# Optimization experiments

Measured on AMD Instinct MI355X. Metric: run time of the kernel, lower is better.

Reference implementation:

```python
import jax, jax.numpy as jnp
import numpy as np

WH, WW = 12, 12
NUM_HEADS = 8
NW = 4


def _relative_position_index():
    ch, cw = np.meshgrid(np.arange(WH), np.arange(WW), indexing='ij')
    coords = np.stack([ch, cw]).reshape(2, -1)            # [2, Wh*Ww]
    rel = coords[:, :, None] - coords[:, None, :]         # [2, M, M]
    rel = rel.transpose(1, 2, 0)                          # [M, M, 2]
    rel[:, :, 0] += WH - 1
    rel[:, :, 1] += WW - 1
    rel[:, :, 0] *= 2 * WW - 1
    return jnp.asarray(rel.sum(-1))                       # [M, M] int


def setup_inputs() -> dict:
    key = jax.random.key(0)
    ks = jax.random.split(key, 11)
    C = 512
    B_, N = 512, WH * WW + 1
    std = 0.02
    return {
        'x': jax.random.normal(ks[0], (B_, N, C), dtype=jnp.float32),
        'mask': jnp.zeros((NW, N, N), dtype=jnp.float32),
        'rpb_table': jax.random.normal(ks[1], ((2 * WH - 1) * (2 * WW - 1), NUM_HEADS), dtype=jnp.float32) * std,
        'Wq': jax.random.normal(ks[2], (C, C), dtype=jnp.float32) * (C ** -0.5),
        'bq': jax.random.normal(ks[3], (C,), dtype=jnp.float32) * std,
        'Wk': jax.random.normal(ks[4], (C, C), dtype=jnp.float32) * (C ** -0.5),
        'bk': jax.random.normal(ks[5], (C,), dtype=jnp.float32) * std,
        'Wv': jax.random.normal(ks[6], (C, C), dtype=jnp.float32) * (C ** -0.5),
        'bv': jax.random.normal(ks[7], (C,), dtype=jnp.float32) * std,
        'Wo': jax.random.normal(ks[8], (C, C), dtype=jnp.float32) * (C ** -0.5),
        'bo': jax.random.normal(ks[9], (C,), dtype=jnp.float32) * std,
    }


def reference(x, mask, rpb_table, Wq, bq, Wk, bk, Wv, bv, Wo, bo):
    B_, N, C = x.shape
    H = NUM_HEADS
    hd = C // H
    scale = hd ** -0.5
    B = B_ // NW
    M = WH * WW  # window tokens (N = M + 1 global token)

    def proj(W, b):
        return (x @ W.T + b).reshape(B_, N, H, hd).transpose(0, 2, 1, 3)  # [B_,H,N,hd]

    q = proj(Wq, bq)
    k = proj(Wk, bk)
    v = proj(Wv, bv)

    attn = jnp.einsum('bhnd,bhmd->bhnm', q, k) * scale  # [B_,H,N,N]

    rel_idx = _relative_position_index()                 # [M,M]
    bias = rpb_table[rel_idx].transpose(2, 0, 1)          # [H,M,M]
    attn = attn.at[:, :, :M, :M].add(bias[None])          # N != M: bias on window block only

    # shifted-window mask: (nW, N, N)
    attn = (attn.reshape(B, NW, H, N, N) + mask[None, :, None]).reshape(B_, H, N, N)

    # ---- global-token attention redistribution (gx) ----
    ga = attn[:, :, -1, :].reshape(B, NW, H, N).transpose(0, 2, 1, 3)   # [B,H,NW,N]
    g1 = ga[:, :, :, :M].reshape(B, H, NW * M)                           # window keys, all windows
    g2 = ga[:, :, :, M].mean(-1, keepdims=True)                          # mean global-global logit [B,H,1]
    g = jax.nn.softmax(jnp.concatenate([g1, g2], axis=-1), axis=-1)      # [B,H,NW*M+1]
    g1 = g[:, :, :-1].reshape(B, H, NW, M).transpose(0, 2, 1, 3).reshape(B_, H, M)
    g2 = jnp.broadcast_to(g[:, :, -1][:, None, :], (B, NW, H)).reshape(B_, H, 1)
    ga_full = jnp.concatenate([g1, g2], axis=-1)[:, :, None, :]          # [B_,H,1,N]
    gx = jnp.einsum('bhqn,bhnd->bhqd', ga_full, v).transpose(0, 2, 1, 3).reshape(B_, C)
    gx = gx.reshape(B, NW, C).sum(1)                                     # sum over windows [B,C]
    gx = jnp.broadcast_to(gx[:, None, :], (B, NW, C)).reshape(B_, C)

    # ---- standard window attention ----
    attn = jax.nn.softmax(attn, axis=-1)
    out = jnp.einsum('bhnm,bhmd->bhnd', attn, v).transpose(0, 2, 1, 3).reshape(B_, N, C)
    out = out.at[:, -1, :].set(gx)
    return out @ Wo.T + bo
```

## Files before the change

kernel.cpp:

```cpp
#include <hip/hip_runtime.h>
#include <hip/hip_bf16.h>
#include <stdint.h>

#define NTOK 145
#define MTOK 144
#define CDIM 512
#define NHEAD 8
#define HD 64
#define NWIN 4
#define BWIN 512
#define MROWS (BWIN*NTOK)

typedef short short8 __attribute__((ext_vector_type(8)));
typedef float f32x4 __attribute__((ext_vector_type(4)));

__device__ __forceinline__ uint16_t f2bf(float f) {
  union { float f; uint32_t u; } x; x.f = f;
  uint32_t r = x.u + 0x7FFFu + ((x.u >> 16) & 1u);
  return (uint16_t)(r >> 16);
}
__device__ __forceinline__ float bf2f(uint16_t u) {
  union { uint32_t u; float f; } x; x.u = ((uint32_t)u) << 16; return x.f;
}
__device__ __forceinline__ uint32_t pack2(float a, float b) {
  return (uint32_t)f2bf(a) | ((uint32_t)f2bf(b) << 16);
}

__global__ void prep_kernel(const float* __restrict__ rpb,
                            const float* __restrict__ Wq, const float* __restrict__ bq,
                            const float* __restrict__ Wk, const float* __restrict__ bk,
                            const float* __restrict__ Wv, const float* __restrict__ bv,
                            const float* __restrict__ Wo,
                            uint16_t* __restrict__ wqkv, uint16_t* __restrict__ wo,
                            float* __restrict__ bqkv, float* __restrict__ biastab) {
  int id = blockIdx.x * 256 + threadIdx.x;
  const int A = 1536*512, B = 512*512, C2 = 1536, D = 8*144*144;
  if (id < A) {
    int n = id >> 9, k = id & 511;
    const float* W = (n < 512) ? Wq : (n < 1024) ? Wk : Wv;
    wqkv[id] = f2bf(W[(size_t)(n & 511)*512 + k]);
  } else if ((id -= A) < B) {
    wo[id] = f2bf(Wo[id]);
  } else if ((id -= B) < C2) {
    bqkv[id] = (id < 512) ? bq[id] : (id < 1024) ? bk[id-512] : bv[id-1024];
  } else if ((id -= C2) < D) {
    int h = id / (144*144); int rr = id % (144*144);
    int i = rr / 144, j = rr % 144;
    int rel = (i/12 - j/12 + 11) * 23 + (i%12 - j%12 + 11);
    biastab[id] = rpb[rel*8 + h];
  }
}

__global__ __launch_bounds__(256) void gemm_qkv(
    const float* __restrict__ x, const uint16_t* __restrict__ wqkv,
    const float* __restrict__ bqkv,
    uint16_t* __restrict__ qb, uint16_t* __restrict__ kb, uint16_t* __restrict__ vb) {
  __shared__ __align__(16) uint16_t As[128*32];
  __shared__ __align__(16) uint16_t Bs[128*32];
  int bid = blockIdx.x;
  int mb = bid / 12, nb = bid % 12;
  int tid = threadIdx.x;
  int lane = tid & 63, w = tid >> 6;
  int wm = w >> 1, wn = w & 1;
  int lm = lane & 15, lq = lane >> 4;
  int sr = tid >> 1, sh = tid & 1;

  const float* agp = x + (size_t)(mb*128 + sr)*512 + sh*16;
  const uint16_t* bgp = wqkv + (size_t)(nb*128 + sr)*512 + sh*16;

  f32x4 acc[4][4];
#pragma unroll
  for (int a = 0; a < 4; a++)
#pragma unroll
    for (int b = 0; b < 4; b++) acc[a][b] = (f32x4){0.f,0.f,0.f,0.f};

  float4 af0 = *(const float4*)(agp+0), af1 = *(const float4*)(agp+4);
  float4 af2 = *(const float4*)(agp+8), af3 = *(const float4*)(agp+12);
  uint4 bu0 = *(const uint4*)(bgp), bu1 = *(const uint4*)(bgp+8);

  for (int kt = 0; kt < 16; kt++) {
    uint32_t p0 = pack2(af0.x, af0.y), p1 = pack2(af0.z, af0.w);
    uint32_t p2 = pack2(af1.x, af1.y), p3 = pack2(af1.z, af1.w);
    uint32_t p4 = pack2(af2.x, af2.y), p5 = pack2(af2.z, af2.w);
    uint32_t p6 = pack2(af3.x, af3.y), p7 = pack2(af3.z, af3.w);
    *(uint4*)&As[sr*32 + sh*16]     = make_uint4(p0,p1,p2,p3);
    *(uint4*)&As[sr*32 + sh*16 + 8] = make_uint4(p4,p5,p6,p7);
    *(uint4*)&Bs[sr*32 + sh*16]     = bu0;
    *(uint4*)&Bs[sr*32 + sh*16 + 8] = bu1;
    __syncthreads();
    if (kt < 15) {
      const float* ag = agp + (kt+1)*32;
      af0 = *(const float4*)(ag+0); af1 = *(const float4*)(ag+4);
      af2 = *(const float4*)(ag+8); af3 = *(const float4*)(ag+12);
      const uint16_t* bg = bgp + (kt+1)*32;
      bu0 = *(const uint4*)(bg); bu1 = *(const uint4*)(bg+8);
    }
    short8 a[4], b[4];
#pragma unroll
    for (int t = 0; t < 4; t++) a[t] = *(short8*)&As[(wm*64 + t*16 + lm)*32 + lq*8];
#pragma unroll
    for (int t = 0; t < 4; t++) b[t] = *(short8*)&Bs[(wn*64 + t*16 + lm)*32 + lq*8];
#pragma unroll
    for (int tm = 0; tm < 4; tm++)
#pragma unroll
      for (int tn = 0; tn < 4; tn++)
        acc[tm][tn] = __builtin_amdgcn_mfma_f32_16x16x32_bf16(a[tm], b[tn], acc[tm][tn], 0, 0, 0);
    __syncthreads();
  }
#pragma unroll
  for (int tn = 0; tn < 4; tn++) {
    int n = nb*128 + wn*64 + tn*16 + lm;
    float bias = bqkv[n];
    int which = n >> 9, c = n & 511;
    uint16_t* dst = (which == 0) ? qb : (which == 1) ? kb : vb;
    int hh = c >> 6, dd = c & 63;
#pragma unroll
    for (int tm = 0; tm < 4; tm++) {
#pragma unroll
      for (int r = 0; r < 4; r++) {
        int m = mb*128 + wm*64 + tm*16 + lq*4 + r;
        int bw = m / 145, nl = m - bw*145;
        dst[((size_t)(bw*8 + hh)*145 + nl)*64 + dd] = f2bf(acc[tm][tn][r] + bias);
      }
    }
  }
}

__global__ __launch_bounds__(256, 2) void attn_kernel(
    const uint16_t* __restrict__ qb, const uint16_t* __restrict__ kb,
    const uint16_t* __restrict__ vb, const float* __restrict__ biastab,
    const float* __restrict__ mask, float* __restrict__ glog,
    uint16_t* __restrict__ attn_out) {
  __shared__ __align__(16) uint16_t P[144*160];
  __shared__ __align__(16) uint16_t vs[145*64];
  int bid = blockIdx.x;
  int b_ = bid >> 3, h = bid & 7;
  int nw = b_ & 3;
  int tid = threadIdx.x, lane = tid & 63, w = tid >> 6;
  int lm = lane & 15, lq = lane >> 4;
  const size_t hbase = ((size_t)(b_*8 + h)) * (145*64);
  const uint16_t* qp = qb + hbase;
  const uint16_t* kp = kb + hbase;
  const uint16_t* vp = vb + hbase;

  for (int c = tid; c < 1160; c += 256)
    *(uint4*)&vs[c*8] = *(const uint4*)(vp + (size_t)c*8);

  int nmt = (w < 2) ? 3 : 2;
  f32x4 acc[3][10];
#pragma unroll
  for (int a = 0; a < 3; a++)
#pragma unroll
    for (int b = 0; b < 10; b++) acc[a][b] = (f32x4){0.f,0.f,0.f,0.f};

#pragma unroll
  for (int ks = 0; ks < 2; ks++) {
    short8 bfr[10];
#pragma unroll
    for (int nt = 0; nt < 10; nt++) {
      int j = nt*16 + lm; if (j > 144) j = 144;
      bfr[nt] = *(const short8*)(kp + (size_t)j*64 + ks*32 + lq*8);
    }
#pragma unroll
    for (int mtl = 0; mtl < 3; mtl++) {
      if (mtl < nmt) {
        int mt = w + mtl*4;
        int i = mt*16 + lm; if (i > 144) i = 144;
        short8 afr = *(const short8*)(qp + (size_t)i*64 + ks*32 + lq*8);
#pragma unroll
        for (int nt = 0; nt < 10; nt++)
          acc[mtl][nt] = __builtin_amdgcn_mfma_f32_16x16x32_bf16(afr, bfr[nt], acc[mtl][nt], 0, 0, 0);
      }
    }
  }

  const float scale = 0.125f;
#pragma unroll
  for (int mtl = 0; mtl < 3; mtl++) {
    if (mtl >= nmt) continue;
    int mt = w + mtl*4;
    if (mt == 9) {
      if (lq == 0) {
#pragma unroll
        for (int nt = 0; nt < 10; nt++) {
          int j = nt*16 + lm;
          if (j < 145)
            glog[(size_t)(b_*8 + h)*145 + j] =
                acc[mtl][nt][0]*scale + mask[(nw*145 + 144)*145 + j];
        }
      }
      continue;
    }
#pragma unroll
    for (int r = 0; r < 4; r++) {
      int i = mt*16 + lq*4 + r;
      float mx = -3.0e38f;
#pragma unroll
      for (int nt = 0; nt < 10; nt++) {
        int j = nt*16 + lm;
        float t = acc[mtl][nt][r]*scale;
        if (j < 145) t += mask[(nw*145 + i)*145 + j];
        if (j < 144) t += biastab[(h*144 + i)*144 + j];
        if (j >= 145) t = -3.0e38f;
        acc[mtl][nt][r] = t;
        mx = fmaxf(mx, t);
      }
#pragma unroll
      for (int off = 1; off < 16; off <<= 1) mx = fmaxf(mx, __shfl_xor(mx, off));
      float sum = 0.f;
#pragma unroll
      for (int nt = 0; nt < 10; nt++) {
        int j = nt*16 + lm;
        float p = (j < 145) ? __expf(acc[mtl][nt][r] - mx) : 0.f;
        acc[mtl][nt][r] = p; sum += p;
      }
#pragma unroll
      for (int off = 1; off < 16; off <<= 1) sum += __shfl_xor(sum, off);
      float rs = __builtin_amdgcn_rcpf(sum);
#pragma unroll
      for (int nt = 0; nt < 10; nt++)
        P[i*160 + nt*16 + lm] = f2bf(acc[mtl][nt][r] * rs);
    }
  }
  __syncthreads();

  f32x4 oacc[9];
#pragma unroll
  for (int a = 0; a < 9; a++) oacc[a] = (f32x4){0.f,0.f,0.f,0.f};
#pragma unroll
  for (int ks = 0; ks < 5; ks++) {
    short8 bfr;
#pragma unroll
    for (int jj = 0; jj < 8; jj++) {
      int j = ks*32 + lq*8 + jj; if (j > 144) j = 144;
      bfr[jj] = (short)vs[j*64 + w*16 + lm];
    }
#pragma unroll
    for (int mt = 0; mt < 9; mt++) {
      short8 afr = *(short8*)&P[(mt*16 + lm)*160 + ks*32 + lq*8];
      oacc[mt] = __builtin_amdgcn_mfma_f32_16x16x32_bf16(afr, bfr, oacc[mt], 0, 0, 0);
    }
  }
#pragma unroll
  for (int mt = 0; mt < 9; mt++) {
#pragma unroll
    for (int r = 0; r < 4; r++) {
      int i = mt*16 + lq*4 + r;
      attn_out[((size_t)b_*145 + i)*512 + h*64 + w*16 + lm] = f2bf(oacc[mt][r]);
    }
  }
}

__global__ __launch_bounds__(64) void gx_kernel(
    const float* __restrict__ glog, const uint16_t* __restrict__ vb,
    uint16_t* __restrict__ attn_out) {
  int bid = blockIdx.x;
  int b = bid >> 3, h = bid & 7;
  int lane = threadIdx.x;
  __shared__ float lg[580];
  __shared__ float pl[576];
  for (int nwi = 0; nwi < 4; nwi++)
    for (int t = lane; t < 145; t += 64)
      lg[nwi*145 + t] = glog[(size_t)((b*4 + nwi)*8 + h)*145 + t];
  __syncthreads();
  float g2 = 0.25f*(lg[144] + lg[289] + lg[434] + lg[579]);
  float mx = g2;
  for (int t = lane; t < 576; t += 64) {
    int nwi = t / 144, j = t - nwi*144;
    mx = fmaxf(mx, lg[nwi*145 + j]);
  }
#pragma unroll
  for (int off = 1; off < 64; off <<= 1) mx = fmaxf(mx, __shfl_xor(mx, off));
  float sum = 0.f;
  for (int t = lane; t < 576; t += 64) {
    int nwi = t / 144, j = t - nwi*144;
    float p = __expf(lg[nwi*145 + j] - mx);
    pl[t] = p; sum += p;
  }
#pragma unroll
  for (int off = 1; off < 64; off <<= 1) sum += __shfl_xor(sum, off);
  float p2 = __expf(g2 - mx);
  float rs = __builtin_amdgcn_rcpf(sum + p2);
  __syncthreads();
  float acc = 0.f;
  int d = lane;
  for (int nwi = 0; nwi < 4; nwi++) {
    const uint16_t* vp = vb + (size_t)((b*4 + nwi)*8 + h)*(145*64);
#pragma unroll 4
    for (int j = 0; j < 144; j++)
      acc += pl[nwi*144 + j] * bf2f(vp[j*64 + d]);
    acc += p2 * bf2f(vp[144*64 + d]);
  }
  acc *= rs;
  uint16_t o = f2bf(acc);
  for (int nwi = 0; nwi < 4; nwi++)
    attn_out[((size_t)(b*4 + nwi)*145 + 144)*512 + h*64 + d] = o;
}

__global__ __launch_bounds__(256) void gemm_out(
    const uint16_t* __restrict__ A, const uint16_t* __restrict__ wo,
    const float* __restrict__ bo, float* __restrict__ out) {
  __shared__ __align__(16) uint16_t As[128*32];
  __shared__ __align__(16) uint16_t Bs[128*32];
  int bid = blockIdx.x;
  int mb = bid >> 2, nb = bid & 3;
  int tid = threadIdx.x;
  int lane = tid & 63, w = tid >> 6;
  int wm = w >> 1, wn = w & 1;
  int lm = lane & 15, lq = lane >> 4;
  int sr = tid >> 1, sh = tid & 1;

  const uint16_t* agp = A + (size_t)(mb*128 + sr)*512 + sh*16;
  const uint16_t* bgp = wo + (size_t)(nb*128 + sr)*512 + sh*16;

  f32x4 acc[4][4];
#pragma unroll
  for (int a = 0; a < 4; a++)
#pragma unroll
    for (int b = 0; b < 4; b++) acc[a][b] = (f32x4){0.f,0.f,0.f,0.f};

  uint4 au0 = *(const uint4*)(agp), au1 = *(const uint4*)(agp+8);
  uint4 bu0 = *(const uint4*)(bgp), bu1 = *(const uint4*)(bgp+8);

  for (int kt = 0; kt < 16; kt++) {
    *(uint4*)&As[sr*32 + sh*16]     = au0;
    *(uint4*)&As[sr*32 + sh*16 + 8] = au1;
    *(uint4*)&Bs[sr*32 + sh*16]     = bu0;
    *(uint4*)&Bs[sr*32 + sh*16 + 8] = bu1;
    __syncthreads();
    if (kt < 15) {
      const uint16_t* ag = agp + (kt+1)*32;
      au0 = *(const uint4*)(ag); au1 = *(const uint4*)(ag+8);
      const uint16_t* bg = bgp + (kt+1)*32;
      bu0 = *(const uint4*)(bg); bu1 = *(const uint4*)(bg+8);
    }
    short8 a[4], b[4];
#pragma unroll
    for (int t = 0; t < 4; t++) a[t] = *(short8*)&As[(wm*64 + t*16 + lm)*32 + lq*8];
#pragma unroll
    for (int t = 0; t < 4; t++) b[t] = *(short8*)&Bs[(wn*64 + t*16 + lm)*32 + lq*8];
#pragma unroll
    for (int tm = 0; tm < 4; tm++)
#pragma unroll
      for (int tn = 0; tn < 4; tn++)
        acc[tm][tn] = __builtin_amdgcn_mfma_f32_16x16x32_bf16(a[tm], b[tn], acc[tm][tn], 0, 0, 0);
    __syncthreads();
  }
#pragma unroll
  for (int tn = 0; tn < 4; tn++) {
    int n = nb*128 + wn*64 + tn*16 + lm;
    float bias = bo[n];
#pragma unroll
    for (int tm = 0; tm < 4; tm++) {
#pragma unroll
      for (int r = 0; r < 4; r++) {
        int m = mb*128 + wm*64 + tm*16 + lq*4 + r;
        out[(size_t)m*512 + n] = acc[tm][tn][r] + bias;
      }
    }
  }
}

extern "C" void kernel_launch(void* const* d_in, const int* in_sizes, int n_in,
                              void* d_out, int out_size, void* d_ws, size_t ws_size,
                              hipStream_t stream) {
  const float* x    = (const float*)d_in[0];
  const float* mask = (const float*)d_in[1];
  const float* rpb  = (const float*)d_in[2];
  const float* Wq   = (const float*)d_in[3];
  const float* bq   = (const float*)d_in[4];
  const float* Wk   = (const float*)d_in[5];
  const float* bk   = (const float*)d_in[6];
  const float* Wv   = (const float*)d_in[7];
  const float* bv   = (const float*)d_in[8];
  const float* Wo   = (const float*)d_in[9];
  const float* bo   = (const float*)d_in[10];

  uint8_t* ws = (uint8_t*)d_ws;
  size_t off = 0;
  auto alloc = [&](size_t bytes) -> void* {
    void* p = ws + off; off += (bytes + 255) & ~(size_t)255; return p;
  };
  uint16_t* wqkv   = (uint16_t*)alloc((size_t)1536*512*2);
  uint16_t* wo     = (uint16_t*)alloc((size_t)512*512*2);
  float*    bqkv   = (float*)alloc(1536*4);
  float*    biastab= (float*)alloc((size_t)8*144*144*4);
  float*    glog   = (float*)alloc((size_t)512*8*145*4);
  uint16_t* qb     = (uint16_t*)alloc((size_t)MROWS*512*2);
  uint16_t* kb     = (uint16_t*)alloc((size_t)MROWS*512*2);
  uint16_t* vb     = (uint16_t*)alloc((size_t)MROWS*512*2);
  uint16_t* attn   = (uint16_t*)alloc((size_t)MROWS*512*2);

  prep_kernel<<<4750, 256, 0, stream>>>(rpb, Wq, bq, Wk, bk, Wv, bv, Wo,
                                        wqkv, wo, bqkv, biastab);
  gemm_qkv<<<580*12, 256, 0, stream>>>(x, wqkv, bqkv, qb, kb, vb);
  attn_kernel<<<4096, 256, 0, stream>>>(qb, kb, vb, biastab, mask, glog, attn);
  gx_kernel<<<1024, 64, 0, stream>>>(glog, vb, attn);
  gemm_out<<<580*4, 256, 0, stream>>>(attn, wo, bo, (float*)d_out);
}
```

Measured before the change: 862.7 us.

## Pre-cast x to bf16, use direct global-to-LDS loads, swizzle GEMM blocks, widen gx

Adds a separate kernel that casts x to bf16 up front, so the QKV GEMM can load both operands with global_load_lds straight into shared memory instead of staging them through registers with conversion. Both GEMMs also remap block indices into groups of 8 M-tiles that share N-tiles, to improve L2 reuse. The gx kernel moves from one wave to four, one wave per window, with cross-wave reductions through shared memory. Costs: an extra pass over x and a bf16 buffer, and the register prefetch of the next K tile is removed, so loads and MFMA no longer overlap within a block.

After: 726.1 us. -15.8%, faster.

```diff
diff --git a/kernel.cpp b/kernel.cpp
--- a/kernel.cpp
+++ b/kernel.cpp
@@ -24,6 +24,18 @@
 }
 __device__ __forceinline__ uint32_t pack2(float a, float b) {
   return (uint32_t)f2bf(a) | ((uint32_t)f2bf(b) << 16);
+}
+
+#define GLL(gp, lp) __builtin_amdgcn_global_load_lds( \
+    (const __attribute__((address_space(1))) uint32_t*)(gp), \
+    (__attribute__((address_space(3))) uint32_t*)(lp), 16, 0, 0)
+
+__global__ __launch_bounds__(256) void cast_x(const float* __restrict__ x,
+                                              uint16_t* __restrict__ xb) {
+  size_t id = ((size_t)blockIdx.x*256 + threadIdx.x)*8;
+  float4 a = *(const float4*)(x+id), c = *(const float4*)(x+id+4);
+  uint4 o = make_uint4(pack2(a.x,a.y), pack2(a.z,a.w), pack2(c.x,c.y), pack2(c.z,c.w));
+  *(uint4*)(xb+id) = o;
 }
 
 __global__ void prep_kernel(const float* __restrict__ rpb,
@@ -52,21 +64,25 @@
 }
 
 __global__ __launch_bounds__(256) void gemm_qkv(
-    const float* __restrict__ x, const uint16_t* __restrict__ wqkv,
+    const uint16_t* __restrict__ xb, const uint16_t* __restrict__ wqkv,
     const float* __restrict__ bqkv,
     uint16_t* __restrict__ qb, uint16_t* __restrict__ kb, uint16_t* __restrict__ vb) {
   __shared__ __align__(16) uint16_t As[128*32];
   __shared__ __align__(16) uint16_t Bs[128*32];
   int bid = blockIdx.x;
-  int mb = bid / 12, nb = bid % 12;
+  int mb, nb;
+  if (bid < 6912) { int g = bid / 96, r = bid % 96; mb = g*8 + (r & 7); nb = r >> 3; }
+  else           { int r = bid - 6912;              mb = 576 + (r & 3); nb = r >> 2; }
   int tid = threadIdx.x;
   int lane = tid & 63, w = tid >> 6;
   int wm = w >> 1, wn = w & 1;
   int lm = lane & 15, lq = lane >> 4;
-  int sr = tid >> 1, sh = tid & 1;
-
-  const float* agp = x + (size_t)(mb*128 + sr)*512 + sh*16;
-  const uint16_t* bgp = wqkv + (size_t)(nb*128 + sr)*512 + sh*16;
+
+  int srow = lane >> 2, scol = (lane & 3) * 8;
+  const uint16_t* agp = xb   + (size_t)(mb*128 + w*32 + srow)*512 + scol;
+  const uint16_t* bgp = wqkv + (size_t)(nb*128 + w*32 + srow)*512 + scol;
+  uint16_t* Asw = &As[w*32*32];
+  uint16_t* Bsw = &Bs[w*32*32];
 
   f32x4 acc[4][4];
 #pragma unroll
@@ -74,27 +90,12 @@
 #pragma unroll
     for (int b = 0; b < 4; b++) acc[a][b] = (f32x4){0.f,0.f,0.f,0.f};
 
-  float4 af0 = *(const float4*)(agp+0), af1 = *(const float4*)(agp+4);
-  float4 af2 = *(const float4*)(agp+8), af3 = *(const float4*)(agp+12);
-  uint4 bu0 = *(const uint4*)(bgp), bu1 = *(const uint4*)(bgp+8);
-
   for (int kt = 0; kt < 16; kt++) {
-    uint32_t p0 = pack2(af0.x, af0.y), p1 = pack2(af0.z, af0.w);
-    uint32_t p2 = pack2(af1.x, af1.y), p3 = pack2(af1.z, af1.w);
-    uint32_t p4 = pack2(af2.x, af2.y), p5 = pack2(af2.z, af2.w);
-    uint32_t p6 = pack2(af3.x, af3.y), p7 = pack2(af3.z, af3.w);
-    *(uint4*)&As[sr*32 + sh*16]     = make_uint4(p0,p1,p2,p3);
-    *(uint4*)&As[sr*32 + sh*16 + 8] = make_uint4(p4,p5,p6,p7);
-    *(uint4*)&Bs[sr*32 + sh*16]     = bu0;
-    *(uint4*)&Bs[sr*32 + sh*16 + 8] = bu1;
+    GLL(agp + kt*32,          Asw);
+    GLL(agp + kt*32 + 16*512, Asw + 16*32);
+    GLL(bgp + kt*32,          Bsw);
+    GLL(bgp + kt*32 + 16*512, Bsw + 16*32);
     __syncthreads();
-    if (kt < 15) {
-      const float* ag = agp + (kt+1)*32;
-      af0 = *(const float4*)(ag+0); af1 = *(const float4*)(ag+4);
-      af2 = *(const float4*)(ag+8); af3 = *(const float4*)(ag+12);
-      const uint16_t* bg = bgp + (kt+1)*32;
-      bu0 = *(const uint4*)(bg); bu1 = *(const uint4*)(bg+8);
-    }
     short8 a[4], b[4];
 #pragma unroll
     for (int t = 0; t < 4; t++) a[t] = *(short8*)&As[(wm*64 + t*16 + lm)*32 + lq*8];
@@ -251,50 +252,60 @@
   }
 }
 
-__global__ __launch_bounds__(64) void gx_kernel(
+__global__ __launch_bounds__(256) void gx_kernel(
     const float* __restrict__ glog, const uint16_t* __restrict__ vb,
     uint16_t* __restrict__ attn_out) {
   int bid = blockIdx.x;
   int b = bid >> 3, h = bid & 7;
-  int lane = threadIdx.x;
+  int tid = threadIdx.x, lane = tid & 63, w = tid >> 6;
   __shared__ float lg[580];
   __shared__ float pl[576];
-  for (int nwi = 0; nwi < 4; nwi++)
-    for (int t = lane; t < 145; t += 64)
-      lg[nwi*145 + t] = glog[(size_t)((b*4 + nwi)*8 + h)*145 + t];
+  __shared__ float sred[8];
+  __shared__ float sacc[256];
+  for (int t = tid; t < 580; t += 256) {
+    int nwi = t / 145, j = t - nwi*145;
+    lg[t] = glog[(size_t)((b*4 + nwi)*8 + h)*145 + j];
+  }
   __syncthreads();
   float g2 = 0.25f*(lg[144] + lg[289] + lg[434] + lg[579]);
   float mx = g2;
-  for (int t = lane; t < 576; t += 64) {
+  for (int t = tid; t < 576; t += 256) {
     int nwi = t / 144, j = t - nwi*144;
     mx = fmaxf(mx, lg[nwi*145 + j]);
   }
 #pragma unroll
   for (int off = 1; off < 64; off <<= 1) mx = fmaxf(mx, __shfl_xor(mx, off));
+  if (lane == 0) sred[w] = mx;
+  __syncthreads();
+  mx = fmaxf(fmaxf(sred[0], sred[1]), fmaxf(sred[2], sred[3]));
   float sum = 0.f;
-  for (int t = lane; t < 576; t += 64) {
+  for (int t = tid; t < 576; t += 256) {
     int nwi = t / 144, j = t - nwi*144;
     float p = __expf(lg[nwi*145 + j] - mx);
     pl[t] = p; sum += p;
   }
 #pragma unroll
   for (int off = 1; off < 64; off <<= 1) sum += __shfl_xor(sum, off);
+  if (lane == 0) sred[4 + w] = sum;
+  __syncthreads();
+  sum = (sred[4] + sred[5]) + (sred[6] + sred[7]);
   float p2 = __expf(g2 - mx);
   float rs = __builtin_amdgcn_rcpf(sum + p2);
-  __syncthreads();
+  const uint16_t* vp = vb + (size_t)((b*4 + w)*8 + h)*(145*64);
   float acc = 0.f;
   int d = lane;
-  for (int nwi = 0; nwi < 4; nwi++) {
-    const uint16_t* vp = vb + (size_t)((b*4 + nwi)*8 + h)*(145*64);
 #pragma unroll 4
-    for (int j = 0; j < 144; j++)
-      acc += pl[nwi*144 + j] * bf2f(vp[j*64 + d]);
-    acc += p2 * bf2f(vp[144*64 + d]);
-  }
-  acc *= rs;
-  uint16_t o = f2bf(acc);
-  for (int nwi = 0; nwi < 4; nwi++)
-    attn_out[((size_t)(b*4 + nwi)*145 + 144)*512 + h*64 + d] = o;
+  for (int j = 0; j < 144; j++)
+    acc += pl[w*144 + j] * bf2f(vp[j*64 + d]);
+  acc += p2 * bf2f(vp[144*64 + d]);
+  sacc[tid] = acc;
+  __syncthreads();
+  if (w == 0) {
+    float tot = (sacc[lane] + sacc[64 + lane]) + (sacc[128 + lane] + sacc[192 + lane]);
+    uint16_t o = f2bf(tot * rs);
+    for (int nwi = 0; nwi < 4; nwi++)
+      attn_out[((size_t)(b*4 + nwi)*145 + 144)*512 + h*64 + d] = o;
+  }
 }
 
 __global__ __launch_bounds__(256) void gemm_out(
@@ -303,15 +314,19 @@
   __shared__ __align__(16) uint16_t As[128*32];
   __shared__ __align__(16) uint16_t Bs[128*32];
   int bid = blockIdx.x;
-  int mb = bid >> 2, nb = bid & 3;
+  int mb, nb;
+  if (bid < 2304) { int g = bid / 32, r = bid % 32; mb = g*8 + (r & 7); nb = r >> 3; }
+  else            { int r = bid - 2304;             mb = 576 + (r & 3); nb = r >> 2; }
   int tid = threadIdx.x;
   int lane = tid & 63, w = tid >> 6;
   int wm = w >> 1, wn = w & 1;
   int lm = lane & 15, lq = lane >> 4;
-  int sr = tid >> 1, sh = tid & 1;
-
-  const uint16_t* agp = A + (size_t)(mb*128 + sr)*512 + sh*16;
-  const uint16_t* bgp = wo + (size_t)(nb*128 + sr)*512 + sh*16;
+
+  int srow = lane >> 2, scol = (lane & 3) * 8;
+  const uint16_t* agp = A  + (size_t)(mb*128 + w*32 + srow)*512 + scol;
+  const uint16_t* bgp = wo + (size_t)(nb*128 + w*32 + srow)*512 + scol;
+  uint16_t* Asw = &As[w*32*32];
+  uint16_t* Bsw = &Bs[w*32*32];
 
   f32x4 acc[4][4];
 #pragma unroll
@@ -319,21 +334,12 @@
 #pragma unroll
     for (int b = 0; b < 4; b++) acc[a][b] = (f32x4){0.f,0.f,0.f,0.f};
 
-  uint4 au0 = *(const uint4*)(agp), au1 = *(const uint4*)(agp+8);
-  uint4 bu0 = *(const uint4*)(bgp), bu1 = *(const uint4*)(bgp+8);
-
   for (int kt = 0; kt < 16; kt++) {
-    *(uint4*)&As[sr*32 + sh*16]     = au0;
-    *(uint4*)&As[sr*32 + sh*16 + 8] = au1;
-    *(uint4*)&Bs[sr*32 + sh*16]     = bu0;
-    *(uint4*)&Bs[sr*32 + sh*16 + 8] = bu1;
+    GLL(agp + kt*32,          Asw);
+    GLL(agp + kt*32 + 16*512, Asw + 16*32);
+    GLL(bgp + kt*32,          Bsw);
+    GLL(bgp + kt*32 + 16*512, Bsw + 16*32);
     __syncthreads();
-    if (kt < 15) {
-      const uint16_t* ag = agp + (kt+1)*32;
-      au0 = *(const uint4*)(ag); au1 = *(const uint4*)(ag+8);
-      const uint16_t* bg = bgp + (kt+1)*32;
-      bu0 = *(const uint4*)(bg); bu1 = *(const uint4*)(bg+8);
-    }
     short8 a[4], b[4];
 #pragma unroll
     for (int t = 0; t < 4; t++) a[t] = *(short8*)&As[(wm*64 + t*16 + lm)*32 + lq*8];
@@ -386,15 +392,17 @@
   float*    bqkv   = (float*)alloc(1536*4);
   float*    biastab= (float*)alloc((size_t)8*144*144*4);
   float*    glog   = (float*)alloc((size_t)512*8*145*4);
+  uint16_t* xb     = (uint16_t*)alloc((size_t)MROWS*512*2);
   uint16_t* qb     = (uint16_t*)alloc((size_t)MROWS*512*2);
   uint16_t* kb     = (uint16_t*)alloc((size_t)MROWS*512*2);
   uint16_t* vb     = (uint16_t*)alloc((size_t)MROWS*512*2);
   uint16_t* attn   = (uint16_t*)alloc((size_t)MROWS*512*2);
 
+  cast_x<<<18560, 256, 0, stream>>>(x, xb);
   prep_kernel<<<4750, 256, 0, stream>>>(rpb, Wq, bq, Wk, bk, Wv, bv, Wo,
                                         wqkv, wo, bqkv, biastab);
-  gemm_qkv<<<580*12, 256, 0, stream>>>(x, wqkv, bqkv, qb, kb, vb);
+  gemm_qkv<<<580*12, 256, 0, stream>>>(xb, wqkv, bqkv, qb, kb, vb);
   attn_kernel<<<4096, 256, 0, stream>>>(qb, kb, vb, biastab, mask, glog, attn);
-  gx_kernel<<<1024, 64, 0, stream>>>(glog, vb, attn);
+  gx_kernel<<<1024, 256, 0, stream>>>(glog, vb, attn);
   gemm_out<<<580*4, 256, 0, stream>>>(attn, wo, bo, (float*)d_out);
 }
```
